# Optimization experiments

Measured on AMD Instinct MI355X. Metric: run time of the kernel, lower is better.

Reference implementation:

```python
import jax, jax.numpy as jnp
import numpy as np
from math import sqrt

# ---- config (mirrors init_kwargs / input_specs) ----
B, N = 2, 2048
DIM, HEADS = 1024, 16
DH = DIM // HEADS
NUM_STEPS = 8
BETA = 1.0
SCALE = sqrt(DIM / 2 - 1)        # scale_from_dim(dim)
SCALE_HEAD = sqrt(DH / 2 - 1)    # scale_from_dim(dim_head)


def _normalize(x, eps=1e-12):
    # torch F.normalize(dim=-1): x / max(||x||, eps)
    n = jnp.linalg.norm(x, axis=-1, keepdims=True)
    return x / jnp.maximum(n, eps)


def _theta(x, J, m):
    # effective field: external field + attention-weighted coupling of magnetizations
    return x + jnp.einsum('bhij,bhjd->bhid', J, m)


def _magnetizations(theta, beta=BETA, scale=SCALE):
    # naive-MF single-site average for a vector spin on a sphere of radius `scale`
    # (steepest-descent closed form): m = beta*theta / (2 t),
    # t = (1 + sqrt(1 + beta^2 |theta|^2 / scale^2)) / 2
    # -> linear response beta*theta/2 for small fields, saturates at |m| = scale.
    h2 = jnp.sum(jnp.square(beta * theta), axis=-1, keepdims=True)
    t = 0.5 * (1.0 + jnp.sqrt(1.0 + h2 / (scale * scale)))
    return beta * theta / (2.0 * t)


def setup_inputs() -> dict:
    key = jax.random.key(0)
    k0, k1, k2, k3 = jax.random.split(key, 4)
    x = jax.random.normal(k0, (B, N, DIM), jnp.float32)
    w_qk = jax.random.normal(k1, (2 * DIM, DIM), jnp.float32) / sqrt(DIM)
    w1 = jax.random.normal(k2, (4 * DIM, DIM), jnp.float32) / sqrt(DIM)
    w2 = jax.random.normal(k3, (DIM, 4 * DIM), jnp.float32) / sqrt(4 * DIM)
    return {"x": x, "w_qk": w_qk, "w1": w1, "w2": w2}


def reference(x, w_qk, w1, w2):
    # pre_mix = Identity
    x = SCALE * _normalize(x)                         # [b,n,dim]
    qk = x @ w_qk.T                                   # [b,n,2*dim]
    q, k = jnp.split(qk, 2, axis=-1)
    ff = jax.nn.gelu(x @ w1.T, approximate=False) @ w2.T

    split = lambda t: t.reshape(B, N, HEADS, DH).transpose(0, 2, 1, 3)  # b h n d
    xh, q, k, ffh = map(split, (x, q, k, ff))
    q, k = _normalize(q), _normalize(k)
    sim = SCALE_HEAD * jnp.einsum('bhid,bhjd->bhij', q, k)
    attn = jax.nn.softmax(sim, axis=-1)               # [b,h,n,n] coupling matrix

    xf = xh + ffh                                     # external field
    # prev_mf_state.theta starts as ones(x.shape) on first call
    m0 = _magnetizations(jnp.ones_like(xf))

    # fixed-step mean-field iteration: m <- magnetizations(theta(x, attn, m))
    def body(m, _):
        m_next = _magnetizations(_theta(xf, attn, m))
        return m_next, None
    m, _ = jax.lax.scan(body, m0, None, length=NUM_STEPS)

    m = m.transpose(0, 2, 1, 3).reshape(B, N, DIM)    # merge heads
    # post_mix = Identity
    return m
```

## Files before the change

### kernel.cpp

```cpp
#include <hip/hip_runtime.h>
#include <hip/hip_bf16.h>
#include <math.h>

#define BQ 2
#define SEQ 2048
#define NDIM 1024
#define HEADS 16
#define DH 64
#define NSTEPS 8
#define SCALE 22.60530911f
#define SCALE_HEAD 5.567764363f
#define INV_SCALE2 (1.0f/511.0f)
#define EXS 8.0325527f

typedef unsigned short u16;
typedef unsigned char u8;
typedef long long i64;
typedef __attribute__((ext_vector_type(8))) short bf16x8;
typedef __attribute__((ext_vector_type(4))) float floatx4;
typedef __attribute__((ext_vector_type(2))) long long i64x2;

__device__ __forceinline__ float bf2f(u16 u) {
  union { unsigned int i; float f; } v; v.i = ((unsigned int)u) << 16; return v.f;
}
__device__ __forceinline__ u16 f2bf(float f) {
  union { float f; unsigned int i; } v; v.f = f;
  unsigned int x = v.i;
  return (u16)((x + 0x7fffu + ((x >> 16) & 1u)) >> 16);
}
#if __has_builtin(__builtin_amdgcn_exp2f)
__device__ __forceinline__ float exp2_raw(float x) { return __builtin_amdgcn_exp2f(x); }
#else
__device__ __forceinline__ float exp2_raw(float x) { return exp2f(x); }
#endif
#if __has_builtin(__builtin_amdgcn_rcpf)
__device__ __forceinline__ float rcp_raw(float x) { return __builtin_amdgcn_rcpf(x); }
#else
__device__ __forceinline__ float rcp_raw(float x) { return 1.0f/x; }
#endif

__device__ __forceinline__ float gelu_tanh(float v) {
  float v2 = v*v;
  float u = v * __builtin_fmaf(0.0356774081f, v2, 0.7978845608f);
  float t = exp2_raw(2.8853900817779268f * u);
  float th = (t - 1.0f) * rcp_raw(t + 1.0f);
  return 0.5f * v * (1.0f + th);
}

__device__ __forceinline__ int pk4_fp8(float a, float b, float c, float d) {
  int p = 0;
  p = __builtin_amdgcn_cvt_pk_fp8_f32(a, b, p, false);
  p = __builtin_amdgcn_cvt_pk_fp8_f32(c, d, p, true);
  return p;
}

#define GLD16(gp, lp) __builtin_amdgcn_global_load_lds( \
    (__attribute__((address_space(1))) void*)(gp),      \
    (__attribute__((address_space(3))) void*)(lp), 16, 0, 0)


__global__ void k_flag0(int* flag) { if (threadIdx.x == 0 && blockIdx.x == 0) *flag = 0; }

__global__ __launch_bounds__(256) void k_probe(const u16* __restrict__ x, int* __restrict__ flag) {
  int i = blockIdx.x * 256 + threadIdx.x;
  float v = bf2f(x[i]);
  if (!(fabsf(v) <= 1e4f)) atomicOr(flag, 1);
}

__global__ __launch_bounds__(256) void k_convert(const void* __restrict__ in, u16* __restrict__ outb,
                                                 const int* __restrict__ flag, int n) {
  int i = blockIdx.x * 256 + threadIdx.x;
  if (i >= n) return;
  if (*flag) outb[i] = f2bf(((const float*)in)[i]);
  else       outb[i] = ((const u16*)in)[i];
}

__global__ __launch_bounds__(256) void k_norm_scale(const u16* __restrict__ x, u16* __restrict__ xs) {
  __shared__ float red[256];
  int row = blockIdx.x;
  const u16* xr = x + (size_t)row * NDIM;
  u16* orow = xs + (size_t)row * NDIM;
  int t = threadIdx.x;
  float vals[4]; float s = 0.f;
#pragma unroll
  for (int e = 0; e < 4; e++) { float v = bf2f(xr[t + 256*e]); vals[e] = v; s += v*v; }
  red[t] = s; __syncthreads();
  for (int o = 128; o > 0; o >>= 1) { if (t < o) red[t] += red[t+o]; __syncthreads(); }
  float sc = SCALE / fmaxf(sqrtf(red[0]), 1e-12f);
#pragma unroll
  for (int e = 0; e < 4; e++) orow[t + 256*e] = f2bf(vals[e] * sc);
}

template<int OUT_BF16, int GELU, int ADDSRC>
__global__ __launch_bounds__(256) void k_gemm(const u16* __restrict__ A, const u16* __restrict__ W,
                                              float* __restrict__ Cf, u16* __restrict__ Cb,
                                              const u16* __restrict__ addsrc, int M, int N, int K) {
  __shared__ __align__(16) u16 As[2][128*32];
  __shared__ __align__(16) u16 Bs[2][128*32];
  int t = threadIdx.x;
  int w = t >> 6, L = t & 63;
  int quad = L >> 4, l15 = L & 15;
  int wr = w >> 1, wc = w & 1;
  int bm = blockIdx.x * 128, bn = blockIdx.y * 128;
  int srow = L >> 2, scol = (L & 3) * 8;
  floatx4 acc[4][4];
#pragma unroll
  for (int i = 0; i < 4; i++)
#pragma unroll
    for (int j = 0; j < 4; j++) acc[i][j] = (floatx4){0.f,0.f,0.f,0.f};

  for (int k0 = 0; k0 < K; k0 += 64) {
#pragma unroll
    for (int c = 0; c < 2; c++) {
      int r = c*64 + w*16 + srow;
      const u16* ap = A + (size_t)(bm + r)*K + k0 + scol;
      const u16* wp = W + (size_t)(bn + r)*K + k0 + scol;
      GLD16(ap,      &As[0][(c*64 + w*16)*32]);
      GLD16(ap + 32, &As[1][(c*64 + w*16)*32]);
      GLD16(wp,      &Bs[0][(c*64 + w*16)*32]);
      GLD16(wp + 32, &Bs[1][(c*64 + w*16)*32]);
    }
    __syncthreads();
#pragma unroll
    for (int s = 0; s < 2; s++) {
      bf16x8 af[4], bfr[4];
#pragma unroll
      for (int mt = 0; mt < 4; mt++) af[mt]  = *(const bf16x8*)&As[s][(wr*64 + mt*16 + l15)*32 + quad*8];
#pragma unroll
      for (int nt = 0; nt < 4; nt++) bfr[nt] = *(const bf16x8*)&Bs[s][(wc*64 + nt*16 + l15)*32 + quad*8];
#pragma unroll
      for (int mt = 0; mt < 4; mt++)
#pragma unroll
        for (int nt = 0; nt < 4; nt++)
          acc[mt][nt] = __builtin_amdgcn_mfma_f32_16x16x32_bf16(af[mt], bfr[nt], acc[mt][nt], 0, 0, 0);
    }
    __syncthreads();
  }
#pragma unroll
  for (int mt = 0; mt < 4; mt++)
#pragma unroll
    for (int reg = 0; reg < 4; reg++) {
      int m = bm + wr*64 + mt*16 + quad*4 + reg;
      size_t rowoff = (size_t)m * N;
#pragma unroll
      for (int nt = 0; nt < 4; nt++) {
        int n = bn + wc*64 + nt*16 + l15;
        float v = acc[mt][nt][reg];
        if (GELU) v = gelu_tanh(v);
        if (ADDSRC) v += bf2f(addsrc[rowoff + n]);
        if (OUT_BF16) Cb[rowoff + n] = f2bf(v);
        else Cf[rowoff + n] = v;
      }
    }
}

__global__ __launch_bounds__(512) void k_gemm_w2(const u16* __restrict__ A, const u16* __restrict__ W,
                                                 float* __restrict__ Cf,
                                                 const u16* __restrict__ addsrc, int M, int N, int K) {
  __shared__ __align__(16) u16 As[2][128*32];
  __shared__ __align__(16) u16 Bs[2][128*32];
  int t = threadIdx.x;
  int g = t >> 8;
  int tg = t & 255;
  int w = tg >> 6;
  int L = t & 63;
  int quad = L >> 4, l15 = L & 15;
  int wr = w >> 1, wc = w & 1;
  int bm = blockIdx.x * 128, bn = blockIdx.y * 128;
  int srow = L >> 2, scol = (L & 3) * 8;
  int kg0 = g * (K >> 1);
  floatx4 acc[4][4];
#pragma unroll
  for (int i = 0; i < 4; i++)
#pragma unroll
    for (int j = 0; j < 4; j++) acc[i][j] = (floatx4){0.f,0.f,0.f,0.f};

  for (int k0 = 0; k0 < (K >> 1); k0 += 32) {
    int kk = kg0 + k0;
#pragma unroll
    for (int c = 0; c < 2; c++) {
      int r = c*64 + w*16 + srow;
      GLD16(A + (size_t)(bm + r)*K + kk + scol, &As[g][(c*64 + w*16)*32]);
      GLD16(W + (size_t)(bn + r)*K + kk + scol, &Bs[g][(c*64 + w*16)*32]);
    }
    __syncthreads();
    bf16x8 af[4], bfr[4];
#pragma unroll
    for (int mt = 0; mt < 4; mt++) af[mt]  = *(const bf16x8*)&As[g][(wr*64 + mt*16 + l15)*32 + quad*8];
#pragma unroll
    for (int nt = 0; nt < 4; nt++) bfr[nt] = *(const bf16x8*)&Bs[g][(wc*64 + nt*16 + l15)*32 + quad*8];
#pragma unroll
    for (int mt = 0; mt < 4; mt++)
#pragma unroll
      for (int nt = 0; nt < 4; nt++)
        acc[mt][nt] = __builtin_amdgcn_mfma_f32_16x16x32_bf16(af[mt], bfr[nt], acc[mt][nt], 0, 0, 0);
    __syncthreads();
  }
  float* LFA = (float*)&As[0][0];
  float* LFB = (float*)&Bs[0][0];
#pragma unroll
  for (int r = 0; r < 2; r++) {
    float* myW = g ? LFA : LFB;
    int mtW = g ? r : (2 + r);
#pragma unroll
    for (int reg = 0; reg < 4; reg++)
#pragma unroll
      for (int nt = 0; nt < 4; nt++)
        myW[(wr*16 + quad*4 + reg)*128 + wc*64 + nt*16 + l15] = acc[mtW][nt][reg];
    __syncthreads();
    float* myR = g ? LFB : LFA;
    int mtS = g ? (2 + r) : r;
#pragma unroll
    for (int reg = 0; reg < 4; reg++) {
      int m = bm + wr*64 + mtS*16 + quad*4 + reg;
      size_t rowoff = (size_t)m * N;
#pragma unroll
      for (int nt = 0; nt < 4; nt++) {
        int n = bn + wc*64 + nt*16 + l15;
        float v = acc[mtS][nt][reg] + myR[(wr*16 + quad*4 + reg)*128 + wc*64 + nt*16 + l15];
        v += bf2f(addsrc[rowoff + n]);
        Cf[rowoff + n] = v;
      }
    }
    __syncthreads();
  }
}

__global__ __launch_bounds__(512) void k_gemm_w2ks(const u16* __restrict__ A, const u16* __restrict__ W,
                                                   float* __restrict__ pbuf, int M, int N, int K) {
  __shared__ __align__(16) u16 As[2][128*32];
  __shared__ __align__(16) u16 Bs[2][128*32];
  int t = threadIdx.x;
  int g = t >> 8;
  int tg = t & 255;
  int w = tg >> 6;
  int L = t & 63;
  int quad = L >> 4, l15 = L & 15;
  int wr = w >> 1, wc = w & 1;
  int bm = blockIdx.x * 128, bn = blockIdx.y * 128;
  int z = blockIdx.z;
  int srow = L >> 2, scol = (L & 3) * 8;
  int kg0 = z * (K >> 1) + g * (K >> 2);
  floatx4 acc[4][4];
#pragma unroll
  for (int i = 0; i < 4; i++)
#pragma unroll
    for (int j = 0; j < 4; j++) acc[i][j] = (floatx4){0.f,0.f,0.f,0.f};

  for (int k0 = 0; k0 < (K >> 2); k0 += 32) {
    int kk = kg0 + k0;
#pragma unroll
    for (int c = 0; c < 2; c++) {
      int r = c*64 + w*16 + srow;
      GLD16(A + (size_t)(bm + r)*K + kk + scol, &As[g][(c*64 + w*16)*32]);
      GLD16(W + (size_t)(bn + r)*K + kk + scol, &Bs[g][(c*64 + w*16)*32]);
    }
    __syncthreads();
    bf16x8 af[4], bfr[4];
#pragma unroll
    for (int mt = 0; mt < 4; mt++) af[mt]  = *(const bf16x8*)&As[g][(wr*64 + mt*16 + l15)*32 + quad*8];
#pragma unroll
    for (int nt = 0; nt < 4; nt++) bfr[nt] = *(const bf16x8*)&Bs[g][(wc*64 + nt*16 + l15)*32 + quad*8];
#pragma unroll
    for (int mt = 0; mt < 4; mt++)
#pragma unroll
      for (int nt = 0; nt < 4; nt++)
        acc[mt][nt] = __builtin_amdgcn_mfma_f32_16x16x32_bf16(af[mt], bfr[nt], acc[mt][nt], 0, 0, 0);
    __syncthreads();
  }
  float* LFA = (float*)&As[0][0];
  float* LFB = (float*)&Bs[0][0];
  float* pb = pbuf + (size_t)z * M * N;
#pragma unroll
  for (int r = 0; r < 2; r++) {
    float* myW = g ? LFA : LFB;
    int mtW = g ? r : (2 + r);
#pragma unroll
    for (int reg = 0; reg < 4; reg++)
#pragma unroll
      for (int nt = 0; nt < 4; nt++)
        myW[(wr*16 + quad*4 + reg)*128 + wc*64 + nt*16 + l15] = acc[mtW][nt][reg];
    __syncthreads();
    float* myR = g ? LFB : LFA;
    int mtS = g ? (2 + r) : r;
#pragma unroll
    for (int reg = 0; reg < 4; reg++) {
      int m = bm + wr*64 + mtS*16 + quad*4 + reg;
      size_t rowoff = (size_t)m * N;
#pragma unroll
      for (int nt = 0; nt < 4; nt++) {
        int n = bn + wc*64 + nt*16 + l15;
        pb[rowoff + n] = acc[mtS][nt][reg] + myR[(wr*16 + quad*4 + reg)*128 + wc*64 + nt*16 + l15];
      }
    }
    __syncthreads();
  }
}

__global__ __launch_bounds__(256) void k_w2red(const float* __restrict__ p0, const float* __restrict__ p1,
                                               const u16* __restrict__ xs, float* __restrict__ xf, int n) {
  int i = (blockIdx.x * 256 + threadIdx.x) * 4;
  if (i >= n) return;
  float4 a = *(const float4*)(p0 + i);
  float4 b = *(const float4*)(p1 + i);
  ushort4 s = *(const ushort4*)(xs + i);
  float4 o;
  o.x = a.x + b.x + bf2f(s.x);
  o.y = a.y + b.y + bf2f(s.y);
  o.z = a.z + b.z + bf2f(s.z);
  o.w = a.w + b.w + bf2f(s.w);
  *(float4*)(xf + i) = o;
}

__global__ __launch_bounds__(64) void k_headnorm(const u16* __restrict__ qkraw,
                                                 u16* __restrict__ qn, u16* __restrict__ kn) {
  int blk = blockIdx.x;
  int h = blk & (HEADS-1); int bi = blk >> 4;
  int b = bi >> 11, i = bi & (SEQ-1);
  int d = threadIdx.x;
  const u16* base = qkraw + (size_t)bi * (2*NDIM);
  float qv = bf2f(base[h*DH + d]);
  float kv = bf2f(base[NDIM + h*DH + d]);
  float qs = qv*qv, ks = kv*kv;
#pragma unroll
  for (int o = 32; o > 0; o >>= 1) { qs += __shfl_xor(qs, o); ks += __shfl_xor(ks, o); }
  size_t oidx = ((size_t)(b*HEADS + h) * SEQ + i) * DH + d;
  qn[oidx] = f2bf(qv / fmaxf(sqrtf(qs), 1e-12f));
  kn[oidx] = f2bf(kv / fmaxf(sqrtf(ks), 1e-12f));
}

__global__ __launch_bounds__(256, 4) void k_attn(const u16* __restrict__ qb, const u16* __restrict__ kb,
                                                 u8* __restrict__ attn, float* __restrict__ rowsum,
                                                 int bh0) {
  __shared__ __align__(16) u8 buf[4][4][64][16];
  __shared__ float reds[4][4][16];
  int t = threadIdx.x;
  int w = t >> 6, L = t & 63;
  int quad = L >> 4, l15 = L & 15;
  int bh_local = blockIdx.x >> 5;
  int bh = bh0 + bh_local;
  int i0blk = (blockIdx.x & 31) * 64;
  bf16x8 q0[4], q1[4];
#pragma unroll
  for (int s = 0; s < 4; s++) {
    const u16* qrow = qb + ((size_t)bh*SEQ + i0blk + s*16 + l15)*DH + quad*8;
    q0[s] = *(const bf16x8*)qrow;
    q1[s] = *(const bf16x8*)(qrow + 32);
  }
  const u16* kbase = kb + (size_t)bh*SEQ*DH;
  u8* abase = attn + ((size_t)bh_local << 22) + (size_t)(i0blk >> 4)*32768;
  float sa[4] = {0.f, 0.f, 0.f, 0.f};
  for (int g = 0; g < 8; g++) {
#pragma unroll 2
    for (int tt4 = 0; tt4 < 4; tt4++) {
      int j = w*512 + (g*4 + tt4)*16 + l15;
      const u16* krow = kbase + (size_t)j*DH + quad*8;
      bf16x8 a0 = *(const bf16x8*)krow;
      bf16x8 a1 = *(const bf16x8*)(krow + 32);
      int dl = ((tt4*2 + (quad>>1)) & 3)*16 + l15;
      int boff = (tt4>>1)*8 + (quad&1)*4;
#pragma unroll
      for (int s = 0; s < 4; s++) {
        floatx4 c = (floatx4){0.f,0.f,0.f,0.f};
        c = __builtin_amdgcn_mfma_f32_16x16x32_bf16(a0, q0[s], c, 0, 0, 0);
        c = __builtin_amdgcn_mfma_f32_16x16x32_bf16(a1, q1[s], c, 0, 0, 0);
        float e0 = exp2_raw(EXS * c[0]);
        float e1 = exp2_raw(EXS * c[1]);
        float e2 = exp2_raw(EXS * c[2]);
        float e3 = exp2_raw(EXS * c[3]);
        sa[s] += (e0 + e1) + (e2 + e3);
        *(int*)&buf[w][s][dl][boff] = pk4_fp8(e0, e1, e2, e3);
      }
    }
#pragma unroll
    for (int s = 0; s < 4; s++) {
      uint4 v = *(const uint4*)&buf[w][s][L][0];
      *(uint4*)(abase + (size_t)s*32768 + (size_t)(w*8 + g)*1024 + (size_t)L*16) = v;
    }
  }
#pragma unroll
  for (int s = 0; s < 4; s++) {
    float v = sa[s];
    v += __shfl_xor(v, 16); v += __shfl_xor(v, 32);
    if (quad == 0) reds[w][s][l15] = v;
  }
  __syncthreads();
  if (t < 64)
    rowsum[(size_t)bh_local*SEQ + i0blk + t] =
        (reds[0][t >> 4][t & 15] + reds[1][t >> 4][t & 15]) +
        (reds[2][t >> 4][t & 15] + reds[3][t >> 4][t & 15]);
}

__global__ void k_zero(float* __restrict__ o, int n) {
  int i = blockIdx.x*256 + threadIdx.x; if (i < n) o[i] = 0.f;
}

__global__ __launch_bounds__(256) void k_step0(const float* __restrict__ xf, u8* __restrict__ mT,
                                               float m0v) {
  __shared__ __align__(16) u8 tile_t[64][72];
  int bh = blockIdx.x >> 5;
  int kt2 = blockIdx.x & 31;
  int i0 = kt2 * 64;
  int b = bh >> 4, h = bh & (HEADS-1);
  int t = threadIdx.x;
  int row = t >> 2, part = t & 3;
  const float* xr = xf + ((size_t)b*SEQ + i0 + row)*NDIM + h*DH + part*16;
  float v[16]; float s = 0.f;
#pragma unroll
  for (int e = 0; e < 16; e++) { float u = xr[e] + m0v; v[e] = u; s += u*u; }
  s += __shfl_xor(s, 1); s += __shfl_xor(s, 2);
  float t2 = 0.5f*(1.0f + sqrtf(1.0f + s * INV_SCALE2));
  float inv = 1.0f/(2.0f*t2);
#pragma unroll
  for (int e = 0; e < 16; e += 4) {
    int p = pk4_fp8(v[e]*inv, v[e+1]*inv, v[e+2]*inv, v[e+3]*inv);
    tile_t[part*16 + e + 0][row] = (u8)(p & 255);
    tile_t[part*16 + e + 1][row] = (u8)((p >> 8) & 255);
    tile_t[part*16 + e + 2][row] = (u8)((p >> 16) & 255);
    tile_t[part*16 + e + 3][row] = (u8)((p >> 24) & 255);
  }
  __syncthreads();
  int nt = t >> 6, Lw = t & 63;
  i64 lo = *(const i64*)&tile_t[nt*16 + (Lw & 15)][(Lw >> 4)*8];
  i64 hi = *(const i64*)&tile_t[nt*16 + (Lw & 15)][32 + (Lw >> 4)*8];
  u8* dst = mT + ((size_t)bh << 17) + ((size_t)(nt*32 + kt2)*64 + Lw)*16;
  *(i64*)dst = lo;
  *(i64*)(dst + 8) = hi;
}

template<int LAST>
__global__ __launch_bounds__(256) void k_step(const u8* __restrict__ attn, const u8* __restrict__ mT_in,
                                              const float* __restrict__ xf,
                                              const float* __restrict__ rowsum,
                                              u8* __restrict__ mT_out,
                                              float* __restrict__ out, int bh0, int CH) {
  int t = threadIdx.x;
  int w = t >> 6, L = t & 63;
  int quad = L >> 4, l15 = L & 15;
  int blk = blockIdx.x;
  int bh_local, I4;
  if (CH >= 8) {
    int gpb = CH >> 3;
    int q = blk >> 3;
    bh_local = (blk & 7) + 8 * (q % gpb);
    I4 = q / gpb;
  } else {
    bh_local = blk >> 5;
    I4 = blk & 31;
  }
  int bh = bh0 + bh_local;
  int I = I4*4 + w;
  int b = bh >> 4, hh = bh & (HEADS-1);
  const u8* ab = attn + ((size_t)bh_local << 22) + (size_t)I*32768 + (size_t)L*16;
  const u8* bb = mT_in + ((size_t)bh << 17) + (size_t)L*16;
  floatx4 acc[4];
#pragma unroll
  for (int j = 0; j < 4; j++) acc[j] = (floatx4){0.f,0.f,0.f,0.f};

#pragma unroll 4
  for (int kt2 = 0; kt2 < 32; kt2++) {
    i64x2 a  = *(const i64x2*)(ab + (size_t)kt2*1024);
    i64x2 b0 = *(const i64x2*)(bb + (size_t)kt2*1024);
    i64x2 b1 = *(const i64x2*)(bb + (size_t)(32 + kt2)*1024);
    i64x2 b2 = *(const i64x2*)(bb + (size_t)(64 + kt2)*1024);
    i64x2 b3 = *(const i64x2*)(bb + (size_t)(96 + kt2)*1024);
    acc[0] = __builtin_amdgcn_mfma_f32_16x16x32_fp8_fp8(a.x, b0.x, acc[0], 0, 0, 0);
    acc[1] = __builtin_amdgcn_mfma_f32_16x16x32_fp8_fp8(a.x, b1.x, acc[1], 0, 0, 0);
    acc[2] = __builtin_amdgcn_mfma_f32_16x16x32_fp8_fp8(a.x, b2.x, acc[2], 0, 0, 0);
    acc[3] = __builtin_amdgcn_mfma_f32_16x16x32_fp8_fp8(a.x, b3.x, acc[3], 0, 0, 0);
    acc[0] = __builtin_amdgcn_mfma_f32_16x16x32_fp8_fp8(a.y, b0.y, acc[0], 0, 0, 0);
    acc[1] = __builtin_amdgcn_mfma_f32_16x16x32_fp8_fp8(a.y, b1.y, acc[1], 0, 0, 0);
    acc[2] = __builtin_amdgcn_mfma_f32_16x16x32_fp8_fp8(a.y, b2.y, acc[2], 0, 0, 0);
    acc[3] = __builtin_amdgcn_mfma_f32_16x16x32_fp8_fp8(a.y, b3.y, acc[3], 0, 0, 0);
  }
  int ibase = I*16 + quad*4;
  float th[4][4]; float invr[4];
#pragma unroll
  for (int reg = 0; reg < 4; reg++) {
    float sinv = 1.0f / rowsum[(size_t)bh_local*SEQ + ibase + reg];
    size_t xoff = ((size_t)b*SEQ + ibase + reg)*NDIM + hh*DH + l15;
    float s = 0.f;
#pragma unroll
    for (int nt = 0; nt < 4; nt++) {
      float v = acc[nt][reg]*sinv + xf[xoff + nt*16];
      th[nt][reg] = v; s += v*v;
    }
    s += __shfl_xor(s, 1); s += __shfl_xor(s, 2); s += __shfl_xor(s, 4); s += __shfl_xor(s, 8);
    float tt2 = 0.5f*(1.0f + sqrtf(1.0f + s * INV_SCALE2));
    invr[reg] = 1.0f/(2.0f*tt2);
  }
  if (LAST) {
#pragma unroll
    for (int reg = 0; reg < 4; reg++) {
      size_t ooff = ((size_t)b*SEQ + ibase + reg)*NDIM + hh*DH + l15;
#pragma unroll
      for (int nt = 0; nt < 4; nt++) out[ooff + nt*16] = th[nt][reg]*invr[reg];
    }
  } else {
    int kt2o = I >> 2;
    int hf = (I >> 1) & 1;
    int lhi = ((I & 1)*2 + (quad >> 1)) & 3;
    u8* ob = mT_out + ((size_t)bh << 17) + (size_t)(lhi*16 + l15)*16 + hf*8 + (quad & 1)*4;
#pragma unroll
    for (int nt = 0; nt < 4; nt++) {
      int p = pk4_fp8(th[nt][0]*invr[0], th[nt][1]*invr[1],
                      th[nt][2]*invr[2], th[nt][3]*invr[3]);
      *(int*)(ob + (size_t)(nt*32 + kt2o)*1024) = p;
    }
  }
}

extern "C" void kernel_launch(void* const* d_in, const int* in_sizes, int n_in,
                              void* d_out, int out_size, void* d_ws, size_t ws_size,
                              hipStream_t stream) {
  const void* x    = d_in[0];
  const void* w_qk = d_in[1];
  const void* w1   = d_in[2];
  const void* w2   = d_in[3];
  float* out = (float*)d_out;

  const size_t E = (size_t)BQ*SEQ*NDIM;
  const int NW_QK = 2*NDIM*NDIM;
  const int NW1   = 4*NDIM*NDIM;
  const int NW2   = 4*NDIM*NDIM;

  char* ws = (char*)d_ws;
  size_t off = 0;
  auto alloc = [&](size_t bytes) { void* p = ws + off; off += (bytes + 255) & ~255ull; return p; };
  int*  flag = (int*)alloc(256);
  u16*  xs  = (u16*)alloc(E*2);
  u16*  qb  = (u16*)alloc(E*2);
  u16*  kb  = (u16*)alloc(E*2);
  float* xf = (float*)alloc(E*4);
  u8*   mT  = (u8*)alloc(E*2);
  float* rsum = (float*)alloc((size_t)BQ*HEADS*SEQ*4);
  u8*   mTa = mT;
  u8*   mTb = mT + E;

  char* S = ws + off;
  size_t availS = (ws_size > off) ? ws_size - off : 0;
  u16* wqkb  = (u16*)(S);
  u16* qkraw = (u16*)(S + 4194304);
  u16* w1b   = (u16*)(S + 20971520);
  u16* w2b   = (u16*)(S + 29360128);
  u16* hbuf  = (u16*)(S + 37748736);
  u8*  attn  = (u8*)(S);
  u16* xb    = (u16*)mT;

  const int rcs[6] = {4096, 2048, 1024, 512, 256, 128};
  int RC = 0;
  for (int i = 0; i < 6; i++)
    if (37748736ull + (size_t)rcs[i]*4096*2 <= availS) { RC = rcs[i]; break; }
  const int chs[6] = {32, 16, 8, 4, 2, 1};
  int CH = 0;
  for (int i = 0; i < 6; i++)
    if ((size_t)chs[i]*SEQ*SEQ <= availS) { CH = chs[i]; break; }
  if (RC == 0 || CH == 0) {
    k_zero<<<(out_size+255)/256, 256, 0, stream>>>(out, out_size);
    return;
  }
  size_t pboff = 37748736ull + (size_t)RC*4096*2;
  int use_ksp = (pboff + (size_t)RC*NDIM*8 <= availS) ? 1 : 0;
  float* pbuf = (float*)(S + pboff);

  const int M = BQ*SEQ;

  k_flag0<<<1, 64, 0, stream>>>(flag);
  k_probe<<<256, 256, 0, stream>>>((const u16*)x, flag);
  k_convert<<<(int)(E/256), 256, 0, stream>>>(x, xb, flag, (int)E);
  k_convert<<<NW_QK/256, 256, 0, stream>>>(w_qk, wqkb, flag, NW_QK);
  k_convert<<<NW1/256, 256, 0, stream>>>(w1, w1b, flag, NW1);
  k_convert<<<NW2/256, 256, 0, stream>>>(w2, w2b, flag, NW2);

  k_norm_scale<<<M, 256, 0, stream>>>(xb, xs);
  { dim3 g(M/128, 2048/128); k_gemm<1,0,0><<<g, 256, 0, stream>>>(xs, wqkb, nullptr, qkraw, nullptr, M, 2048, 1024); }
  k_headnorm<<<M*HEADS, 64, 0, stream>>>(qkraw, qb, kb);

  for (int c = 0; c < M/RC; c++) {
    const u16* xsc = xs + (size_t)c*RC*NDIM;
    { dim3 g(RC/128, 4096/128); k_gemm<1,1,0><<<g, 256, 0, stream>>>(xsc, w1b, nullptr, hbuf, nullptr, RC, 4096, 1024); }
    if (use_ksp) {
      dim3 g(RC/128, 1024/128, 2);
      k_gemm_w2ks<<<g, 512, 0, stream>>>(hbuf, w2b, pbuf, RC, 1024, 4096);
      int n = RC*NDIM;
      k_w2red<<<n/1024, 256, 0, stream>>>(pbuf, pbuf + n, xsc, xf + (size_t)c*RC*NDIM, n);
    } else {
      dim3 g(RC/128, 1024/128);
      k_gemm_w2<<<g, 512, 0, stream>>>(hbuf, w2b, xf + (size_t)c*RC*NDIM, xsc, RC, 1024, 4096);
    }
  }

  float t0 = 0.5f*(1.0f + sqrtf(1.0f + 64.0f/511.0f));
  float m0v = 1.0f/(2.0f*t0);
  k_step0<<<BQ*HEADS*32, 256, 0, stream>>>(xf, mTa, m0v);

  for (int c0 = 0; c0 < BQ*HEADS; c0 += CH) {
    k_attn<<<CH*32, 256, 0, stream>>>(qb, kb, attn, rsum, c0);
    for (int s = 1; s < NSTEPS; s++) {
      u8* src = (s & 1) ? mTa : mTb;
      u8* dst = (s & 1) ? mTb : mTa;
      if (s == NSTEPS-1)
        k_step<1><<<CH*32, 256, 0, stream>>>(attn, src, xf, rsum, nullptr, out, c0, CH);
      else
        k_step<0><<<CH*32, 256, 0, stream>>>(attn, src, xf, rsum, dst, nullptr, c0, CH);
    }
  }
}
```

Before: 519.5 us.

## Fuse mean-field steps into persistent kernel keeping attention tiles in LDS

When the whole attention matrix fits in the workspace, the seven per-step launches are replaced by one persistent kernel per group of 8 heads. Each block loads its 32 KB-per-wave slice of the fp8 attention matrix into shared memory once and reuses it across all iterations. Blocks of the same head synchronise between steps through an agent-scope atomic counter and spin-wait. This removes repeated global reads of the attention matrix and the launch overhead. The risks are deadlock if the 512 blocks are not all co-resident, plus spin-wait costs and low occupancy from 64 KB of LDS per block.

```diff
diff --git a/kernel.cpp b/kernel.cpp
--- a/kernel.cpp
+++ b/kernel.cpp
@@ -426,6 +426,96 @@
   u8* dst = mT + ((size_t)bh << 17) + ((size_t)(nt*32 + kt2)*64 + Lw)*16;
   *(i64*)dst = lo;
   *(i64*)(dst + 8) = hi;
+}
+
+__global__ __launch_bounds__(128) void k_steps(const u8* __restrict__ attn,
+                                               const float* __restrict__ xf,
+                                               const float* __restrict__ rowsum,
+                                               u8* __restrict__ mTa, u8* __restrict__ mTb,
+                                               float* __restrict__ out, int bh0,
+                                               int* __restrict__ ctr) {
+  __shared__ __align__(16) u8 at[65536];
+  int t = threadIdx.x;
+  int w = t >> 6, L = t & 63;
+  int quad = L >> 4, l15 = L & 15;
+  int bh_local = blockIdx.x & 7;
+  int slice = blockIdx.x >> 3;
+  int bh = bh0 + bh_local;
+  int I = slice*2 + w;
+  int b = bh >> 4, hh = bh & (HEADS-1);
+  const u8* ab = attn + ((size_t)bh << 22) + (size_t)I*32768;
+  for (int it = 0; it < 32; it++)
+    GLD16(ab + (size_t)it*1024 + (size_t)L*16, &at[w*32768 + it*1024]);
+  __syncthreads();
+
+  const u8* bbA = mTa + ((size_t)bh << 17) + (size_t)L*16;
+  const u8* bbB = mTb + ((size_t)bh << 17) + (size_t)L*16;
+  int ibase = I*16 + quad*4;
+  for (int s = 1; s < NSTEPS; s++) {
+    const u8* bb = (s & 1) ? bbA : bbB;
+    floatx4 acc[4];
+#pragma unroll
+    for (int j = 0; j < 4; j++) acc[j] = (floatx4){0.f,0.f,0.f,0.f};
+#pragma unroll 4
+    for (int kt2 = 0; kt2 < 32; kt2++) {
+      i64x2 a  = *(const i64x2*)&at[w*32768 + kt2*1024 + L*16];
+      i64x2 b0 = *(const i64x2*)(bb + (size_t)kt2*1024);
+      i64x2 b1 = *(const i64x2*)(bb + (size_t)(32 + kt2)*1024);
+      i64x2 b2 = *(const i64x2*)(bb + (size_t)(64 + kt2)*1024);
+      i64x2 b3 = *(const i64x2*)(bb + (size_t)(96 + kt2)*1024);
+      acc[0] = __builtin_amdgcn_mfma_f32_16x16x32_fp8_fp8(a.x, b0.x, acc[0], 0, 0, 0);
+      acc[1] = __builtin_amdgcn_mfma_f32_16x16x32_fp8_fp8(a.x, b1.x, acc[1], 0, 0, 0);
+      acc[2] = __builtin_amdgcn_mfma_f32_16x16x32_fp8_fp8(a.x, b2.x, acc[2], 0, 0, 0);
+      acc[3] = __builtin_amdgcn_mfma_f32_16x16x32_fp8_fp8(a.x, b3.x, acc[3], 0, 0, 0);
+      acc[0] = __builtin_amdgcn_mfma_f32_16x16x32_fp8_fp8(a.y, b0.y, acc[0], 0, 0, 0);
+      acc[1] = __builtin_amdgcn_mfma_f32_16x16x32_fp8_fp8(a.y, b1.y, acc[1], 0, 0, 0);
+      acc[2] = __builtin_amdgcn_mfma_f32_16x16x32_fp8_fp8(a.y, b2.y, acc[2], 0, 0, 0);
+      acc[3] = __builtin_amdgcn_mfma_f32_16x16x32_fp8_fp8(a.y, b3.y, acc[3], 0, 0, 0);
+    }
+    float th[4][4]; float invr[4];
+#pragma unroll
+    for (int reg = 0; reg < 4; reg++) {
+      float sinv = 1.0f / rowsum[(size_t)bh*SEQ + ibase + reg];
+      size_t xoff = ((size_t)b*SEQ + ibase + reg)*NDIM + hh*DH + l15;
+      float sq = 0.f;
+#pragma unroll
+      for (int nt = 0; nt < 4; nt++) {
+        float v = acc[nt][reg]*sinv + xf[xoff + nt*16];
+        th[nt][reg] = v; sq += v*v;
+      }
+      sq += __shfl_xor(sq, 1); sq += __shfl_xor(sq, 2); sq += __shfl_xor(sq, 4); sq += __shfl_xor(sq, 8);
+      float tt2 = 0.5f*(1.0f + sqrtf(1.0f + sq * INV_SCALE2));
+      invr[reg] = 1.0f/(2.0f*tt2);
+    }
+    if (s == NSTEPS-1) {
+#pragma unroll
+      for (int reg = 0; reg < 4; reg++) {
+        size_t ooff = ((size_t)b*SEQ + ibase + reg)*NDIM + hh*DH + l15;
+#pragma unroll
+        for (int nt = 0; nt < 4; nt++) out[ooff + nt*16] = th[nt][reg]*invr[reg];
+      }
+    } else {
+      u8* dst = (s & 1) ? mTb : mTa;
+      int kt2o = I >> 2;
+      int hf = (I >> 1) & 1;
+      int lhi = ((I & 1)*2 + (quad >> 1)) & 3;
+      u8* ob = dst + ((size_t)bh << 17) + (size_t)(lhi*16 + l15)*16 + hf*8 + (quad & 1)*4;
+#pragma unroll
+      for (int nt = 0; nt < 4; nt++) {
+        int p = pk4_fp8(th[nt][0]*invr[0], th[nt][1]*invr[1],
+                        th[nt][2]*invr[2], th[nt][3]*invr[3]);
+        *(int*)(ob + (size_t)(nt*32 + kt2o)*1024) = p;
+      }
+      __threadfence();
+      __syncthreads();
+      if (t == 0) {
+        __hip_atomic_fetch_add(&ctr[bh_local], 1, __ATOMIC_RELEASE, __HIP_MEMORY_SCOPE_AGENT);
+        while (__hip_atomic_load(&ctr[bh_local], __ATOMIC_ACQUIRE, __HIP_MEMORY_SCOPE_AGENT) < 64*s)
+          __builtin_amdgcn_s_sleep(8);
+      }
+      __syncthreads();
+    }
+  }
 }
 
 template<int LAST>
@@ -534,6 +624,7 @@
   float* xf = (float*)alloc(E*4);
   u8*   mT  = (u8*)alloc(E*2);
   float* rsum = (float*)alloc((size_t)BQ*HEADS*SEQ*4);
+  int*  ctr = (int*)alloc(256);
   u8*   mTa = mT;
   u8*   mTb = mT + E;
 
@@ -594,15 +685,22 @@
   float m0v = 1.0f/(2.0f*t0);
   k_step0<<<BQ*HEADS*32, 256, 0, stream>>>(xf, mTa, m0v);
 
-  for (int c0 = 0; c0 < BQ*HEADS; c0 += CH) {
-    k_attn<<<CH*32, 256, 0, stream>>>(qb, kb, attn, rsum, c0);
-    for (int s = 1; s < NSTEPS; s++) {
-      u8* src = (s & 1) ? mTa : mTb;
-      u8* dst = (s & 1) ? mTb : mTa;
-      if (s == NSTEPS-1)
-        k_step<1><<<CH*32, 256, 0, stream>>>(attn, src, xf, rsum, nullptr, out, c0, CH);
-      else
-        k_step<0><<<CH*32, 256, 0, stream>>>(attn, src, xf, rsum, dst, nullptr, c0, CH);
-    }
-  }
-}
+  if (CH == 32) {
+    k_attn<<<32*32, 256, 0, stream>>>(qb, kb, attn, rsum, 0);
+    k_zero<<<1, 64, 0, stream>>>((float*)ctr, 64);
+    for (int g = 0; g < 4; g++)
+      k_steps<<<512, 128, 0, stream>>>(attn, xf, rsum, mTa, mTb, out, g*8, ctr + g*8);
+  } else {
+    for (int c0 = 0; c0 < BQ*HEADS; c0 += CH) {
+      k_attn<<<CH*32, 256, 0, stream>>>(qb, kb, attn, rsum, c0);
+      for (int s = 1; s < NSTEPS; s++) {
+        u8* src = (s & 1) ? mTa : mTb;
+        u8* dst = (s & 1) ? mTb : mTa;
+        if (s == NSTEPS-1)
+          k_step<1><<<CH*32, 256, 0, stream>>>(attn, src, xf, rsum, nullptr, out, c0, CH);
+        else
+          k_step<0><<<CH*32, 256, 0, stream>>>(attn, src, xf, rsum, dst, nullptr, c0, CH);
+      }
+    }
+  }
+}
```

Measured after the change: 1.756 ms. 3.38x slower.
